# Performance work log

Measured on AMD Instinct MI355X. Metric: run time of the kernel, lower is better.

The kernel has to match this reference:

```python
import jax, jax.numpy as jnp
import numpy as np

NUM_POINTS = 200000
VIEW_NUM = 1
SCALE = 0.05
BIN_RES = 0.01
NUM_BINS = 512
T0 = 0.0
DECAY = 2.0


def setup_inputs() -> dict:
    key = jax.random.key(0)
    k = jax.random.split(key, 6)
    means = jax.random.normal(k[0], (NUM_POINTS, 3), dtype=jnp.float32)
    scan_point = jax.random.normal(k[1], (3,), dtype=jnp.float32)
    # learned params, initialized as in __init__ plus small noise for non-degenerate grads
    colours = 0.01 * jnp.ones((NUM_POINTS, 1), jnp.float32) + 0.001 * jax.random.normal(k[2], (NUM_POINTS, 1), jnp.float32)
    coefficients = 0.1 * jax.random.normal(k[3], (NUM_POINTS, 1), dtype=jnp.float32)
    opacities = 0.1 * jnp.ones((NUM_POINTS, VIEW_NUM), jnp.float32) + 0.01 * jax.random.normal(k[4], (NUM_POINTS, VIEW_NUM), jnp.float32)
    scales = jnp.float32(np.log(SCALE)) * jnp.ones((NUM_POINTS, 1), jnp.float32) + 0.1 * jax.random.normal(k[5], (NUM_POINTS, 1), jnp.float32)
    return {"means": means, "scan_point": scan_point, "colours": colours,
            "coefficients": coefficients, "opacities": opacities, "scales": scales,
            "view_id": 0}


def reference(means, scan_point, colours, coefficients, opacities, scales, view_id):
    # render_conf_hist2: confocal time-of-flight histogram, no rasterization
    intensity = (opacities[:, view_id] ** 2) * (colours[:, 0] ** 2)          # [N]
    coeff = jax.nn.sigmoid(coefficients)                                     # [N,1]
    r0 = jnp.linalg.norm(means - scan_point[None, :], axis=1, keepdims=True) # [N,1]
    r_ = T0 / 2 + (BIN_RES / 2) * jnp.arange(1, NUM_BINS + 1, dtype=jnp.float32)  # [B]
    r = r_[None, :]                                                          # [1,B]
    sigma = jnp.maximum(jnp.mean(jnp.exp(scales), axis=1, keepdims=True), BIN_RES / 2)  # [N,1]
    diff = r - r0                                                            # [N,B]
    e = jnp.exp(-0.5 * (diff / sigma) ** 2)                                  # [N,B]
    pdf1 = np.sqrt(0.5 / np.pi) * e / sigma
    pdf2 = diff * e / (sigma * sigma)
    pdf = coeff * pdf1 + (1.0 - coeff) * pdf2
    pr = jnp.clip(pdf * (BIN_RES / 2), 0.0, 1.0)
    hist = jnp.sum(intensity[:, None] * pr, axis=0)                          # [B]
    return hist / jnp.power(r_, DECAY)
```

## Files before the change

### kernel.cpp

```cpp
#include <hip/hip_runtime.h>
#include <hip/hip_bf16.h>
#include <math.h>


#define NBINS 512
#define CHUNK 256
#define K_SQRT_HALF_PI 0.3989422804014327f
#define LOG2E 1.4426950408889634f

#if __has_builtin(__builtin_amdgcn_exp2f)
#define FAST_EXP2(x) __builtin_amdgcn_exp2f(x)
#else
#define FAST_EXP2(x) __expf((x) * 0.6931471805599453f)
#endif

__global__ __launch_bounds__(NBINS) void gauss_hist(
    const float* __restrict__ means,
    const float* __restrict__ scan_point,
    const float* __restrict__ colours,
    const float* __restrict__ coeffs,
    const float* __restrict__ opac,
    const float* __restrict__ scales,
    const int* __restrict__ view_id,
    float* __restrict__ out,
    int n)
{
    __shared__ float4 s_pt[CHUNK];
    const int t = threadIdx.x;
    const int base = blockIdx.x * CHUNK;

    if (t < CHUNK) {
        const int p = base + t;
        float4 v = make_float4(0.f, 0.f, 0.f, 0.f);
        if (p < n) {
            const int vid = view_id[0];
            float dx = means[3 * p + 0] - scan_point[0];
            float dy = means[3 * p + 1] - scan_point[1];
            float dz = means[3 * p + 2] - scan_point[2];
            float r0 = sqrtf(fmaf(dx, dx, fmaf(dy, dy, dz * dz)));
            float sg = fmaxf(expf(scales[p]), 0.005f);
            float inv_s = 1.0f / sg;
            float coeff = 1.0f / (1.0f + expf(-coeffs[p]));
            float op  = opac[p + vid];
            float col = colours[p];
            float inten = (op * op) * (col * col);
            float ia = inten * 0.005f;
            v.x = r0;
            v.y = -0.5f * inv_s * inv_s * LOG2E;
            v.z = ia * coeff * K_SQRT_HALF_PI * inv_s;
            v.w = ia * (1.0f - coeff) * inv_s * inv_s;
        }
        s_pt[t] = v;
    }
    __syncthreads();

    const float r = 0.005f * (float)(t + 1);
    float acc = 0.f;
#pragma unroll 8
    for (int k = 0; k < CHUNK; ++k) {
        float4 v = s_pt[k];
        float diff = r - v.x;
        float e = FAST_EXP2(diff * diff * v.y);
        acc += __saturatef(e * fmaf(v.w, diff, v.z));
    }
    atomicAdd(&out[t], acc / (r * r));
}

extern "C" void kernel_launch(void* const* d_in, const int* in_sizes, int n_in,
                              void* d_out, int out_size, void* d_ws, size_t ws_size,
                              hipStream_t stream) {
    const float* means = (const float*)d_in[0];
    const float* scan  = (const float*)d_in[1];
    const float* col   = (const float*)d_in[2];
    const float* cf    = (const float*)d_in[3];
    const float* op    = (const float*)d_in[4];
    const float* sc    = (const float*)d_in[5];
    const int*   vid   = (const int*)d_in[6];
    float* out = (float*)d_out;

    const int n = in_sizes[2];
    hipMemsetAsync(d_out, 0, (size_t)out_size * sizeof(float), stream);
    const int blocks = (n + CHUNK - 1) / CHUNK;
    gauss_hist<<<blocks, NBINS, 0, stream>>>(means, scan, col, cf, op, sc, vid, out, n);
}
```

Before: 101.5 us.

## Expand Gaussian exponent into quadratic, two bins per thread, separate partial reduction

The exponent (r-r0)^2*alpha is expanded into a quadratic in r with per-point precomputed coefficients, and the weight becomes a linear function of r. This cuts the inner-loop math to FMAs plus exp2. Each 256-thread block now covers two bins per thread, so every shared-memory load is reused twice. The per-block atomics are replaced by partial rows written to workspace and summed by a second reduce kernel. The quadratic expansion can lose precision through cancellation when r and r0 are large, and the change adds an extra launch and a partials write and read.

```diff
diff --git a/kernel.cpp b/kernel.cpp
--- a/kernel.cpp
+++ b/kernel.cpp
@@ -5,16 +5,19 @@
 
 #define NBINS 512
 #define CHUNK 256
+#define NTHREADS 256
 #define K_SQRT_HALF_PI 0.3989422804014327f
 #define LOG2E 1.4426950408889634f
 
+__device__ __forceinline__ float fast_exp2(float x) {
 #if __has_builtin(__builtin_amdgcn_exp2f)
-#define FAST_EXP2(x) __builtin_amdgcn_exp2f(x)
+    return __builtin_amdgcn_exp2f(x);
 #else
-#define FAST_EXP2(x) __expf((x) * 0.6931471805599453f)
+    return exp2f(x);
 #endif
+}
 
-__global__ __launch_bounds__(NBINS) void gauss_hist(
+__global__ __launch_bounds__(NTHREADS) void gauss_partial(
     const float* __restrict__ means,
     const float* __restrict__ scan_point,
     const float* __restrict__ colours,
@@ -22,16 +25,18 @@
     const float* __restrict__ opac,
     const float* __restrict__ scales,
     const int* __restrict__ view_id,
-    float* __restrict__ out,
+    float* __restrict__ partials,
     int n)
 {
-    __shared__ float4 s_pt[CHUNK];
+    __shared__ float4 s_q[CHUNK];
+    __shared__ float  s_a[CHUNK];
     const int t = threadIdx.x;
     const int base = blockIdx.x * CHUNK;
 
-    if (t < CHUNK) {
+    {
         const int p = base + t;
-        float4 v = make_float4(0.f, 0.f, 0.f, 0.f);
+        float4 q = make_float4(0.f, 0.f, 0.f, 0.f);
+        float a5 = 0.f;
         if (p < n) {
             const int vid = view_id[0];
             float dx = means[3 * p + 0] - scan_point[0];
@@ -43,27 +48,52 @@
             float coeff = 1.0f / (1.0f + expf(-coeffs[p]));
             float op  = opac[p + vid];
             float col = colours[p];
-            float inten = (op * op) * (col * col);
-            float ia = inten * 0.005f;
-            v.x = r0;
-            v.y = -0.5f * inv_s * inv_s * LOG2E;
-            v.z = ia * coeff * K_SQRT_HALF_PI * inv_s;
-            v.w = ia * (1.0f - coeff) * inv_s * inv_s;
+            float ia  = (op * op) * (col * col) * 0.005f;
+            float alpha = -0.5f * inv_s * inv_s * LOG2E;
+            float bw = ia * (1.0f - coeff) * inv_s * inv_s;
+            float aw = ia * coeff * K_SQRT_HALF_PI * inv_s;
+            q.x = alpha;
+            q.y = -2.0f * alpha * r0;
+            q.z = alpha * r0 * r0;
+            q.w = bw;
+            a5  = fmaf(-bw, r0, aw);
         }
-        s_pt[t] = v;
+        s_q[t] = q;
+        s_a[t] = a5;
     }
     __syncthreads();
 
-    const float r = 0.005f * (float)(t + 1);
+    const float ra = 0.005f * (float)(t + 1);
+    const float rb = 0.005f * (float)(t + 1 + 256);
+    const float ra2 = ra * ra, rb2 = rb * rb;
+    float acca = 0.f, accb = 0.f;
+#pragma unroll 4
+    for (int k = 0; k < CHUNK; ++k) {
+        float4 q = s_q[k];
+        float a5 = s_a[k];
+        float arga = fmaf(q.y, ra, fmaf(q.x, ra2, q.z));
+        float argb = fmaf(q.y, rb, fmaf(q.x, rb2, q.z));
+        float ea = fast_exp2(arga);
+        float eb = fast_exp2(argb);
+        float wa = fmaf(q.w, ra, a5);
+        float wb = fmaf(q.w, rb, a5);
+        acca += __saturatef(ea * wa);
+        accb += __saturatef(eb * wb);
+    }
+    float* row = partials + (size_t)blockIdx.x * NBINS;
+    row[t]       = acca;
+    row[t + 256] = accb;
+}
+
+__global__ __launch_bounds__(NBINS) void gauss_reduce(
+    const float* __restrict__ partials, float* __restrict__ out, int nrows)
+{
+    const int bin = threadIdx.x;
     float acc = 0.f;
-#pragma unroll 8
-    for (int k = 0; k < CHUNK; ++k) {
-        float4 v = s_pt[k];
-        float diff = r - v.x;
-        float e = FAST_EXP2(diff * diff * v.y);
-        acc += __saturatef(e * fmaf(v.w, diff, v.z));
-    }
-    atomicAdd(&out[t], acc / (r * r));
+    for (int i = blockIdx.x; i < nrows; i += gridDim.x)
+        acc += partials[(size_t)i * NBINS + bin];
+    const float r = 0.005f * (float)(bin + 1);
+    atomicAdd(&out[bin], acc / (r * r));
 }
 
 extern "C" void kernel_launch(void* const* d_in, const int* in_sizes, int n_in,
@@ -77,9 +107,12 @@
     const float* sc    = (const float*)d_in[5];
     const int*   vid   = (const int*)d_in[6];
     float* out = (float*)d_out;
+    float* partials = (float*)d_ws;
 
     const int n = in_sizes[2];
+    const int blocks = (n + CHUNK - 1) / CHUNK;
+
     hipMemsetAsync(d_out, 0, (size_t)out_size * sizeof(float), stream);
-    const int blocks = (n + CHUNK - 1) / CHUNK;
-    gauss_hist<<<blocks, NBINS, 0, stream>>>(means, scan, col, cf, op, sc, vid, out, n);
+    gauss_partial<<<blocks, NTHREADS, 0, stream>>>(means, scan, col, cf, op, sc, vid, partials, n);
+    gauss_reduce<<<16, NBINS, 0, stream>>>(partials, out, blocks);
 }
```

After: 114.8 us. +13.1%, slower.

## Switch from per-bin gather to per-point windowed scatter into shared histogram

Applied to the files above, without the earlier changes.

Replaces the gather loop, where every bin evaluated every point in a chunk, with a scatter loop: each thread handles one point and visits only the bins between where the pdf clips to zero and eight sigma above r0. Contributions go into a block-level shared-memory histogram through LDS atomics, and each nonzero bin is flushed to global memory once per block. This removes most of the exp evaluations for bins far from each point's radius. In exchange it adds shared-atomic contention, uneven loop lengths across a wavefront, and drops the Gaussian tail beyond eight sigma.

```diff
diff --git a/kernel.cpp b/kernel.cpp
--- a/kernel.cpp
+++ b/kernel.cpp
@@ -4,17 +4,19 @@
 
 
 #define NBINS 512
-#define CHUNK 256
+#define TPB 512
 #define K_SQRT_HALF_PI 0.3989422804014327f
 #define LOG2E 1.4426950408889634f
 
+__device__ __forceinline__ float fast_exp2(float x) {
 #if __has_builtin(__builtin_amdgcn_exp2f)
-#define FAST_EXP2(x) __builtin_amdgcn_exp2f(x)
+    return __builtin_amdgcn_exp2f(x);
 #else
-#define FAST_EXP2(x) __expf((x) * 0.6931471805599453f)
+    return exp2f(x);
 #endif
+}
 
-__global__ __launch_bounds__(NBINS) void gauss_hist(
+__global__ __launch_bounds__(TPB) void gauss_scatter(
     const float* __restrict__ means,
     const float* __restrict__ scan_point,
     const float* __restrict__ colours,
@@ -25,45 +27,49 @@
     float* __restrict__ out,
     int n)
 {
-    __shared__ float4 s_pt[CHUNK];
+    __shared__ float hist[NBINS];
     const int t = threadIdx.x;
-    const int base = blockIdx.x * CHUNK;
+    hist[t] = 0.f;
+    __syncthreads();
 
-    if (t < CHUNK) {
-        const int p = base + t;
-        float4 v = make_float4(0.f, 0.f, 0.f, 0.f);
-        if (p < n) {
-            const int vid = view_id[0];
-            float dx = means[3 * p + 0] - scan_point[0];
-            float dy = means[3 * p + 1] - scan_point[1];
-            float dz = means[3 * p + 2] - scan_point[2];
-            float r0 = sqrtf(fmaf(dx, dx, fmaf(dy, dy, dz * dz)));
-            float sg = fmaxf(expf(scales[p]), 0.005f);
-            float inv_s = 1.0f / sg;
-            float coeff = 1.0f / (1.0f + expf(-coeffs[p]));
-            float op  = opac[p + vid];
-            float col = colours[p];
-            float inten = (op * op) * (col * col);
-            float ia = inten * 0.005f;
-            v.x = r0;
-            v.y = -0.5f * inv_s * inv_s * LOG2E;
-            v.z = ia * coeff * K_SQRT_HALF_PI * inv_s;
-            v.w = ia * (1.0f - coeff) * inv_s * inv_s;
+    const int p = blockIdx.x * TPB + t;
+    if (p < n) {
+        const int vid = view_id[0];
+        float dx = means[3 * p + 0] - scan_point[0];
+        float dy = means[3 * p + 1] - scan_point[1];
+        float dz = means[3 * p + 2] - scan_point[2];
+        float r0 = sqrtf(fmaf(dx, dx, fmaf(dy, dy, dz * dz)));
+        float sg = fmaxf(expf(scales[p]), 0.005f);
+        float inv_s = 1.0f / sg;
+        float coeff = 1.0f / (1.0f + expf(-coeffs[p]));
+        float op  = opac[p + vid];
+        float col = colours[p];
+        float ia  = (op * op) * (col * col) * 0.005f;
+        float nalpha = 0.5f * LOG2E * inv_s * inv_s;
+        float aw = ia * coeff * K_SQRT_HALF_PI * inv_s;
+        float bw = ia * (1.0f - coeff) * inv_s * inv_s;
+
+        float rlo = r0 - aw / bw;
+        float rhi = fmaf(8.0f, sg, r0);
+        int lo = (int)floorf(rlo * 200.f) - 1;
+        int hi = (int)floorf(rhi * 200.f);
+        lo = lo < 0 ? 0 : lo;
+        hi = hi > NBINS - 1 ? NBINS - 1 : hi;
+        for (int b = lo; b <= hi; ++b) {
+            float r = 0.005f * (float)(b + 1);
+            float diff = r - r0;
+            float e = fast_exp2(-(nalpha * diff) * diff);
+            float w = fmaf(bw, diff, aw);
+            atomicAdd(&hist[b], __saturatef(e * w));
         }
-        s_pt[t] = v;
     }
     __syncthreads();
 
-    const float r = 0.005f * (float)(t + 1);
-    float acc = 0.f;
-#pragma unroll 8
-    for (int k = 0; k < CHUNK; ++k) {
-        float4 v = s_pt[k];
-        float diff = r - v.x;
-        float e = FAST_EXP2(diff * diff * v.y);
-        acc += __saturatef(e * fmaf(v.w, diff, v.z));
+    float h = hist[t];
+    if (h != 0.f) {
+        float r = 0.005f * (float)(t + 1);
+        atomicAdd(&out[t], h / (r * r));
     }
-    atomicAdd(&out[t], acc / (r * r));
 }
 
 extern "C" void kernel_launch(void* const* d_in, const int* in_sizes, int n_in,
@@ -80,6 +86,6 @@
 
     const int n = in_sizes[2];
     hipMemsetAsync(d_out, 0, (size_t)out_size * sizeof(float), stream);
-    const int blocks = (n + CHUNK - 1) / CHUNK;
-    gauss_hist<<<blocks, NBINS, 0, stream>>>(means, scan, col, cf, op, sc, vid, out, n);
+    const int blocks = (n + TPB - 1) / TPB;
+    gauss_scatter<<<blocks, TPB, 0, stream>>>(means, scan, col, cf, op, sc, vid, out, n);
 }
```

Result: faster. 90.92 us (-10.4%).
